# Optimization experiments

Measured on AMD Instinct MI355X. Metric: run time of the kernel, lower is better.

The kernel has to match this reference:

```python
import jax, jax.numpy as jnp
import numpy as np

H, N, D, K = 4, 512, 64, 64  # n_heads, node_num, d_model, sparse_k
TEMP = 0.5
EPS = 1e-10


def setup_inputs() -> dict:
    key = jax.random.key(0)
    k1, k2, k3 = jax.random.split(key, 3)
    feats = jax.random.normal(k1, (H, N, D), jnp.float32)
    # torch Linear init ~ U(-1/sqrt(fan_in), 1/sqrt(fan_in)); Gaussian scale is fine for a baseline
    W_out = jax.random.normal(k2, (2 * D, D), jnp.float32) * (1.0 / np.sqrt(2 * D))
    b_out = jnp.zeros((D,), jnp.float32)
    W_cat = jax.random.normal(k3, (D, 2), jnp.float32) * (1.0 / np.sqrt(D))
    b_cat = jnp.zeros((2,), jnp.float32)
    return {"feats": feats, "W_out": W_out, "b_out": b_out,
            "W_cat": W_cat, "b_cat": b_cat, "sparse_k": K}


def reference(feats, W_out, b_out, W_cat, b_cat, sparse_k):
    H_, N_, D_ = feats.shape
    E = N_ * N_
    e = jnp.arange(E)
    rec_idx = e // N_   # receiver node of edge e (rel_rec one-hot gather)
    snd_idx = e % N_    # sender node of edge e (rel_send one-hot gather)
    # cat([senders, receivers], -1): [H, E, 2D]
    x = jnp.concatenate([feats[:, snd_idx], feats[:, rec_idx]], axis=-1)
    h = jax.nn.relu(x @ W_out + b_out)          # [H, E, D]
    logits = h @ W_cat + b_cat                  # [H, E, 2]
    # gumbel-softmax, hard (straight-through)
    U = jax.random.uniform(jax.random.key(42), logits.shape, jnp.float32)
    g = -jnp.log(-jnp.log(U + EPS) + EPS)
    y_soft = jax.nn.softmax((logits + g) / TEMP, axis=-1)
    y_hard = jax.nn.one_hot(jnp.argmax(y_soft, axis=-1), 2, dtype=y_soft.dtype)
    y = jax.lax.stop_gradient(y_hard - y_soft) + y_soft
    connection_matrix = y[..., 1].reshape(H_, N_, N_)
    connection_prob = jax.nn.softmax(logits, axis=-1)[..., 1]  # [H, E]
    _, top_idx = jax.lax.top_k(connection_prob, sparse_k)      # top-k over edges per head
    sparse_labels = jnp.zeros_like(connection_prob).at[
        jnp.arange(H_)[:, None], top_idx].set(1.0)
    return connection_matrix, connection_prob, sparse_labels
```

## Files before the change

### kernel.cpp

```cpp
#include <hip/hip_runtime.h>
#include <stdint.h>

#define H_ 4
#define N_ 512
#define D_ 64
#define E_ (N_ * N_)
#define HE_ (H_ * E_)
#define EPS_ 1e-10f

__device__ __forceinline__ void tf2x32(unsigned x0, unsigned x1,
                                       unsigned& o0, unsigned& o1) {
  const unsigned ks0 = 0u;
  const unsigned ks1 = 42u;
  const unsigned ks2 = 0x1BD11BDAu ^ ks0 ^ ks1;
  x0 += ks0; x1 += ks1;
#define TFR(r) { x0 += x1; x1 = (x1 << (r)) | (x1 >> (32 - (r))); x1 ^= x0; }
  TFR(13) TFR(15) TFR(26) TFR(6)
  x0 += ks1; x1 += ks2 + 1u;
  TFR(17) TFR(29) TFR(16) TFR(24)
  x0 += ks2; x1 += ks0 + 2u;
  TFR(13) TFR(15) TFR(26) TFR(6)
  x0 += ks0; x1 += ks1 + 3u;
  TFR(17) TFR(29) TFR(16) TFR(24)
  x0 += ks1; x1 += ks2 + 4u;
  TFR(13) TFR(15) TFR(26) TFR(6)
  x0 += ks2; x1 += ks0 + 5u;
#undef TFR
  o0 = x0; o1 = x1;
}

__device__ __forceinline__ unsigned rng_bits(unsigned j) {
  unsigned a, b;
  tf2x32(0u, j, a, b);
  return a ^ b;
}

__device__ __forceinline__ float u01(unsigned bits) {
  return __uint_as_float((bits >> 9) | 0x3f800000u) - 1.0f;
}

__global__ __launch_bounds__(256) void precompute_ab(
    const float* __restrict__ feats, const float* __restrict__ W_out,
    float* __restrict__ A, float* __restrict__ B,
    unsigned* __restrict__ cnt, unsigned* __restrict__ done) {
  int row = blockIdx.x * 4 + (threadIdx.x >> 6);
  int d = threadIdx.x & 63;
  if (blockIdx.x == 0) {
    if (threadIdx.x < 4) cnt[threadIdx.x] = 0u;
    else if (threadIdx.x < 8) done[threadIdx.x - 4] = 0u;
  }
  __shared__ float f[4][64];
  f[threadIdx.x >> 6][d] = feats[row * D_ + d];
  __syncthreads();
  const float* fr = f[threadIdx.x >> 6];
  float a = 0.f, b = 0.f;
#pragma unroll 8
  for (int k = 0; k < D_; ++k) {
    float fv = fr[k];
    a = fmaf(fv, W_out[k * D_ + d], a);
    b = fmaf(fv, W_out[(k + D_) * D_ + d], b);
  }
  A[row * D_ + d] = a;
  B[row * D_ + d] = b;
}

__global__ __launch_bounds__(256, 4) void edge_kernel(
    const float* __restrict__ A, const float* __restrict__ B,
    const float* __restrict__ b_out, const float* __restrict__ W_cat,
    const float* __restrict__ b_cat, float* __restrict__ out,
    unsigned long long* __restrict__ blockmax) {
  __shared__ __align__(16) float Ash[64][68];
  __shared__ __align__(16) float Bsh[16][64];
  __shared__ float4 bsh4[16];
  __shared__ float4 wc4[32];
  __shared__ float bc2[2];
  __shared__ unsigned long long wmax[4];

  const int t = threadIdx.x;
  const int h = blockIdx.z;
  const int snd_base = blockIdx.x * 64;
  const int rec_base = blockIdx.y * 16;

  {
    const float4* A4 = (const float4*)(A + (h * N_ + snd_base) * D_);
    for (int i = t; i < 1024; i += 256)
      *(float4*)&Ash[i >> 4][(i & 15) << 2] = A4[i];
    const float4* B4 = (const float4*)(B + (h * N_ + rec_base) * D_);
    *(float4*)&Bsh[t >> 4][(t & 15) << 2] = B4[t];
  }
  if (t < 16) bsh4[t] = ((const float4*)b_out)[t];
  else if (t < 48) wc4[t - 16] = ((const float4*)W_cat)[t - 16];
  else if (t == 48) { bc2[0] = b_cat[0]; bc2[1] = b_cat[1]; }
  __syncthreads();

  const int s = t & 63;
  const int rg = (t >> 6) * 4;

  float l0[4], l1[4];
#pragma unroll
  for (int r = 0; r < 4; ++r) { l0[r] = 0.f; l1[r] = 0.f; }

#pragma unroll
  for (int d4 = 0; d4 < 16; ++d4) {
    const float4 a0 = *(const float4*)&Ash[s][d4 << 2];
    const float4 bd = bsh4[d4];
    const float4 wA = wc4[2 * d4];
    const float4 wB = wc4[2 * d4 + 1];
#pragma unroll
    for (int r = 0; r < 4; ++r) {
      const float4 bv = *(const float4*)&Bsh[rg + r][d4 << 2];
      float t0;
      t0 = fmaxf((a0.x + bv.x) + bd.x, 0.f);
      l0[r] = fmaf(t0, wA.x, l0[r]); l1[r] = fmaf(t0, wA.y, l1[r]);
      t0 = fmaxf((a0.y + bv.y) + bd.y, 0.f);
      l0[r] = fmaf(t0, wA.z, l0[r]); l1[r] = fmaf(t0, wA.w, l1[r]);
      t0 = fmaxf((a0.z + bv.z) + bd.z, 0.f);
      l0[r] = fmaf(t0, wB.x, l0[r]); l1[r] = fmaf(t0, wB.y, l1[r]);
      t0 = fmaxf((a0.w + bv.w) + bd.w, 0.f);
      l0[r] = fmaf(t0, wB.z, l0[r]); l1[r] = fmaf(t0, wB.w, l1[r]);
    }
  }

  unsigned long long mk = 0ull;
#pragma unroll
  for (int r = 0; r < 4; ++r) {
    float L0 = l0[r] + bc2[0];
    float L1 = l1[r] + bc2[1];
    const unsigned snd = (unsigned)(snd_base + s);
    const unsigned rec = (unsigned)(rec_base + rg + r);
    const unsigned e = rec * (unsigned)N_ + snd;
    const unsigned base = ((unsigned)h << 18) + e;
    const unsigned j0 = base * 2u;

    float uu0 = u01(rng_bits(j0));
    float uu1 = u01(rng_bits(j0 + 1u));
    float g0 = -logf(-logf(uu0 + EPS_) + EPS_);
    float g1 = -logf(-logf(uu1 + EPS_) + EPS_);

    float cm = ((L1 + g1) > (L0 + g0)) ? 1.0f : 0.0f;

    float lm = fmaxf(L0, L1);
    float p0 = expf(L0 - lm), p1 = expf(L1 - lm);
    float pr = p1 / (p0 + p1);

    out[base] = cm;
    out[HE_ + base] = pr;

    unsigned long long key =
        ((unsigned long long)__float_as_uint(pr) << 32) | (unsigned)(~e);
    mk = key > mk ? key : mk;
  }

#pragma unroll
  for (int off = 32; off; off >>= 1) {
    unsigned long long o = __shfl_xor(mk, off, 64);
    mk = o > mk ? o : mk;
  }
  if ((t & 63) == 0) wmax[t >> 6] = mk;
  __syncthreads();
  if (t == 0) {
    unsigned long long m = wmax[0];
#pragma unroll
    for (int i = 1; i < 4; ++i) m = wmax[i] > m ? wmax[i] : m;
    blockmax[h * 256 + blockIdx.y * gridDim.x + blockIdx.x] = m;
  }
}

__global__ __launch_bounds__(512) void topk_fused(
    const float* __restrict__ prob, const unsigned long long* __restrict__ blockmax,
    unsigned* __restrict__ cnt, unsigned* __restrict__ done,
    unsigned long long* __restrict__ cand, float* __restrict__ sparse) {
  __shared__ unsigned long long keys[512];
  __shared__ unsigned long long thrS;
  __shared__ unsigned tkS;
  const int t = threadIdx.x, h = blockIdx.y, blk = blockIdx.x;

  if (t < 256) keys[t] = blockmax[h * 256 + t];
  __syncthreads();
  if (t < 256) {
    unsigned long long my = keys[t];
    int rank = 0;
    for (int j = 0; j < 256; ++j) rank += (keys[j] > my);
    if (rank == 63) thrS = my;
  }
  __syncthreads();
  const unsigned long long thr = thrS;

  const unsigned seg = (unsigned)blk * 4096u;
  {
    float4* sp4 = (float4*)(sparse + (unsigned)h * E_ + seg);
    const float4 z = make_float4(0.f, 0.f, 0.f, 0.f);
#pragma unroll
    for (int i = 0; i < 2; ++i) sp4[t + i * 512] = z;
  }
#pragma unroll
  for (int i = 0; i < 2; ++i) {
    const unsigned e0 = seg + (unsigned)i * 2048u + (unsigned)t * 4u;
    float4 p = *(const float4*)(prob + (unsigned)h * E_ + e0);
    float pv[4] = {p.x, p.y, p.z, p.w};
#pragma unroll
    for (int k2 = 0; k2 < 4; ++k2) {
      unsigned e = e0 + (unsigned)k2;
      unsigned long long key =
          ((unsigned long long)__float_as_uint(pv[k2]) << 32) | (unsigned)(~e);
      if (key >= thr) {
        unsigned pos = atomicAdd(&cnt[h], 1u);
        if (pos < 512u) cand[h * 512 + pos] = key;
      }
    }
  }
  __syncthreads();
  if (t == 0) { __threadfence(); tkS = atomicAdd(&done[h], 1u); }
  __syncthreads();

  if (tkS == 63u) {
    if (t == 0) __threadfence();
    __syncthreads();
    unsigned n = atomicAdd(&cnt[h], 0u);
    if (n > 512u) n = 512u;
    unsigned long long my = (t < (int)n) ? cand[h * 512 + t] : 0ull;
    keys[t] = my;
    __syncthreads();
    int rank = 0;
#pragma unroll 8
    for (int j = 0; j < 512; ++j) rank += (keys[j] > my);
    if (my != 0ull && rank < 64) {
      unsigned e = ~(unsigned)(my & 0xFFFFFFFFull);
      if (e < (unsigned)E_) sparse[(unsigned)h * E_ + e] = 1.0f;
    }
  }
}

extern "C" void kernel_launch(void* const* d_in, const int* in_sizes, int n_in,
                              void* d_out, int out_size, void* d_ws, size_t ws_size,
                              hipStream_t stream) {
  const float* feats = (const float*)d_in[0];
  const float* W_out = (const float*)d_in[1];
  const float* b_out = (const float*)d_in[2];
  const float* W_cat = (const float*)d_in[3];
  const float* b_cat = (const float*)d_in[4];
  float* out = (float*)d_out;

  float* A = (float*)d_ws;
  float* B = A + H_ * N_ * D_;
  unsigned long long* blockmax = (unsigned long long*)(B + H_ * N_ * D_);
  unsigned long long* cand = blockmax + H_ * 256;
  unsigned* cnt = (unsigned*)(cand + H_ * 512);
  unsigned* done = cnt + H_;

  precompute_ab<<<dim3(H_ * N_ / 4), dim3(256), 0, stream>>>(feats, W_out, A, B,
                                                             cnt, done);
  edge_kernel<<<dim3(N_ / 64, N_ / 16, H_), dim3(256), 0, stream>>>(
      A, B, b_out, W_cat, b_cat, out, blockmax);
  topk_fused<<<dim3(64, H_), dim3(512), 0, stream>>>(out + HE_, blockmax, cnt,
                                                     done, cand, out + 2 * HE_);
}
```

Before: 112.1 us.

## Split edge kernel into logits pass and separate Gumbel/softmax pass

Breaks the fused edge kernel into two kernels. The first computes the two logits per edge and writes them to an 8 MB workspace buffer. The second reads them back and does the Threefry RNG, Gumbel noise, softmax, output stores and per-block max reduction with 1024-thread blocks. This likely aims to separate the FMA-heavy stage from the transcendental/RNG-heavy stage so each gets better occupancy and coalesced stores. In exchange it adds a global round trip of the logits and one more kernel launch.

```diff
diff --git a/kernel.cpp b/kernel.cpp
--- a/kernel.cpp
+++ b/kernel.cpp
@@ -64,17 +64,15 @@
   B[row * D_ + d] = b;
 }
 
-__global__ __launch_bounds__(256, 4) void edge_kernel(
+__global__ __launch_bounds__(256, 4) void logits_kernel(
     const float* __restrict__ A, const float* __restrict__ B,
     const float* __restrict__ b_out, const float* __restrict__ W_cat,
-    const float* __restrict__ b_cat, float* __restrict__ out,
-    unsigned long long* __restrict__ blockmax) {
+    const float* __restrict__ b_cat, float2* __restrict__ Lp) {
   __shared__ __align__(16) float Ash[64][68];
   __shared__ __align__(16) float Bsh[16][64];
   __shared__ float4 bsh4[16];
   __shared__ float4 wc4[32];
   __shared__ float bc2[2];
-  __shared__ unsigned long long wmax[4];
 
   const int t = threadIdx.x;
   const int h = blockIdx.z;
@@ -121,36 +119,46 @@
     }
   }
 
-  unsigned long long mk = 0ull;
 #pragma unroll
   for (int r = 0; r < 4; ++r) {
-    float L0 = l0[r] + bc2[0];
-    float L1 = l1[r] + bc2[1];
-    const unsigned snd = (unsigned)(snd_base + s);
-    const unsigned rec = (unsigned)(rec_base + rg + r);
-    const unsigned e = rec * (unsigned)N_ + snd;
-    const unsigned base = ((unsigned)h << 18) + e;
-    const unsigned j0 = base * 2u;
-
-    float uu0 = u01(rng_bits(j0));
-    float uu1 = u01(rng_bits(j0 + 1u));
-    float g0 = -logf(-logf(uu0 + EPS_) + EPS_);
-    float g1 = -logf(-logf(uu1 + EPS_) + EPS_);
-
-    float cm = ((L1 + g1) > (L0 + g0)) ? 1.0f : 0.0f;
-
-    float lm = fmaxf(L0, L1);
-    float p0 = expf(L0 - lm), p1 = expf(L1 - lm);
-    float pr = p1 / (p0 + p1);
-
-    out[base] = cm;
-    out[HE_ + base] = pr;
-
-    unsigned long long key =
-        ((unsigned long long)__float_as_uint(pr) << 32) | (unsigned)(~e);
-    mk = key > mk ? key : mk;
-  }
-
+    const float L0 = l0[r] + bc2[0];
+    const float L1 = l1[r] + bc2[1];
+    const unsigned e = (unsigned)(rec_base + rg + r) * (unsigned)N_ +
+                       (unsigned)(snd_base + s);
+    Lp[((unsigned)h << 18) + e] = make_float2(L0, L1);
+  }
+}
+
+__global__ __launch_bounds__(1024, 8) void gumbel_kernel(
+    const float2* __restrict__ Lp, float* __restrict__ out,
+    unsigned long long* __restrict__ blockmax) {
+  __shared__ unsigned long long wmax[16];
+  const int t = threadIdx.x;
+  const unsigned h = blockIdx.y;
+  const unsigned e = (unsigned)blockIdx.x * 1024u + (unsigned)t;
+  const unsigned base = (h << 18) + e;
+
+  const float2 lp = Lp[base];
+  const float L0 = lp.x;
+  const float L1 = lp.y;
+  const unsigned j0 = base * 2u;
+
+  float uu0 = u01(rng_bits(j0));
+  float uu1 = u01(rng_bits(j0 + 1u));
+  float g0 = -logf(-logf(uu0 + EPS_) + EPS_);
+  float g1 = -logf(-logf(uu1 + EPS_) + EPS_);
+
+  float cm = ((L1 + g1) > (L0 + g0)) ? 1.0f : 0.0f;
+
+  float lm = fmaxf(L0, L1);
+  float p0 = expf(L0 - lm), p1 = expf(L1 - lm);
+  float pr = p1 / (p0 + p1);
+
+  out[base] = cm;
+  out[HE_ + base] = pr;
+
+  unsigned long long mk =
+      ((unsigned long long)__float_as_uint(pr) << 32) | (unsigned)(~e);
 #pragma unroll
   for (int off = 32; off; off >>= 1) {
     unsigned long long o = __shfl_xor(mk, off, 64);
@@ -161,8 +169,8 @@
   if (t == 0) {
     unsigned long long m = wmax[0];
 #pragma unroll
-    for (int i = 1; i < 4; ++i) m = wmax[i] > m ? wmax[i] : m;
-    blockmax[h * 256 + blockIdx.y * gridDim.x + blockIdx.x] = m;
+    for (int i = 1; i < 16; ++i) m = wmax[i] > m ? wmax[i] : m;
+    blockmax[h * 256 + blockIdx.x] = m;
   }
 }
 
@@ -243,15 +251,18 @@
 
   float* A = (float*)d_ws;
   float* B = A + H_ * N_ * D_;
-  unsigned long long* blockmax = (unsigned long long*)(B + H_ * N_ * D_);
+  float2* Lp = (float2*)(B + H_ * N_ * D_);
+  unsigned long long* blockmax = (unsigned long long*)(Lp + HE_);
   unsigned long long* cand = blockmax + H_ * 256;
   unsigned* cnt = (unsigned*)(cand + H_ * 512);
   unsigned* done = cnt + H_;
 
   precompute_ab<<<dim3(H_ * N_ / 4), dim3(256), 0, stream>>>(feats, W_out, A, B,
                                                              cnt, done);
-  edge_kernel<<<dim3(N_ / 64, N_ / 16, H_), dim3(256), 0, stream>>>(
-      A, B, b_out, W_cat, b_cat, out, blockmax);
+  logits_kernel<<<dim3(N_ / 64, N_ / 16, H_), dim3(256), 0, stream>>>(
+      A, B, b_out, W_cat, b_cat, Lp);
+  gumbel_kernel<<<dim3(E_ / 1024, H_), dim3(1024), 0, stream>>>(Lp, out,
+                                                                blockmax);
   topk_fused<<<dim3(64, H_), dim3(512), 0, stream>>>(out + HE_, blockmax, cnt,
                                                      done, cand, out + 2 * HE_);
 }
```

New measurement: 114.6 us. 1.02x slower.

## Fuse the three launches into one cooperative kernel with grid barriers

Applied to the files above, without the earlier changes.

Replaces the precompute, edge and top-k launches with a single cooperative mega-kernel of 1024 workgroups. Phases are separated by a custom grid barrier built on 16 spread-out atomic counters with sleep polling. The goal is to remove per-launch overhead and gaps between kernels, and the zeroing of sparse labels now overlaps with the A/B precompute. In exchange it adds a memset launch and grid-wide barrier latency, and depends on all 1024 blocks being co-resident; if the cooperative launch fails it falls back to the old three-kernel path.

```diff
diff --git a/kernel.cpp b/kernel.cpp
--- a/kernel.cpp
+++ b/kernel.cpp
@@ -7,6 +7,7 @@
 #define E_ (N_ * N_)
 #define HE_ (H_ * E_)
 #define EPS_ 1e-10f
+#define NWG_ 1024ull
 
 __device__ __forceinline__ void tf2x32(unsigned x0, unsigned x1,
                                        unsigned& o0, unsigned& o1) {
@@ -39,6 +40,217 @@
   return __uint_as_float((bits >> 9) | 0x3f800000u) - 1.0f;
 }
 
+#define GBAR(PH)                                                          \
+  do {                                                                    \
+    __syncthreads();                                                      \
+    if (t == 0) {                                                         \
+      __threadfence();                                                    \
+      atomicAdd(&bar[(bl & 15) << 4], 1ull);                              \
+      const unsigned long long _tgt = (unsigned long long)(PH)*NWG_;      \
+      for (long _i = 0; _i < 2000000L; ++_i) {                            \
+        unsigned long long _s = 0ull;                                     \
+        _Pragma("unroll")                                                 \
+        for (int _k = 0; _k < 16; ++_k)                                   \
+          _s += __hip_atomic_load(&bar[_k << 4], __ATOMIC_RELAXED,        \
+                                  __HIP_MEMORY_SCOPE_AGENT);              \
+        if (_s >= _tgt) break;                                            \
+        __builtin_amdgcn_s_sleep(4);                                      \
+      }                                                                   \
+      __threadfence();                                                    \
+    }                                                                     \
+    __syncthreads();                                                      \
+  } while (0)
+
+__global__ __launch_bounds__(256, 4) void mega_kernel(
+    const float* __restrict__ feats, const float* __restrict__ W_out,
+    const float* __restrict__ b_out, const float* __restrict__ W_cat,
+    const float* __restrict__ b_cat, float* __restrict__ out,
+    float* __restrict__ A, float* __restrict__ B,
+    unsigned long long* __restrict__ blockmax,
+    unsigned long long* __restrict__ cand, unsigned* __restrict__ cnt,
+    unsigned long long* __restrict__ bar) {
+  __shared__ __align__(16) float Ash[64][68];
+  __shared__ __align__(16) float Bsh[16][64];
+  __shared__ float4 bsh4[16];
+  __shared__ float4 wc4[32];
+  __shared__ float bc2[2];
+  __shared__ unsigned long long wmax[4];
+  __shared__ unsigned long long thrS;
+
+  const int t = threadIdx.x;
+  const int bl = blockIdx.x;
+  const int bx = bl & 7, by = (bl >> 3) & 31, h = bl >> 8;
+  const int snd_base = bx * 64;
+  const int rec_base = by * 16;
+
+  if (bl == 0 && t < 4) cnt[t] = 0u;
+  {
+    ((float4*)(out + 2 * HE_ + ((unsigned)h << 18) + (unsigned)(bl & 255) * 1024u))[t] =
+        make_float4(0.f, 0.f, 0.f, 0.f);
+
+    const int g = t >> 6;
+    const int d = t & 63;
+    const int row = bl * 2 + (g & 1);
+    float* fsh = &Ash[0][0];
+    if (g < 2) fsh[(g << 6) + d] = feats[row * D_ + d];
+    __syncthreads();
+    if (g < 2) {
+      const float* fr = &fsh[g << 6];
+      float a = 0.f, b = 0.f;
+#pragma unroll 8
+      for (int k = 0; k < D_; ++k) {
+        float fv = fr[k];
+        a = fmaf(fv, W_out[k * D_ + d], a);
+        b = fmaf(fv, W_out[(k + D_) * D_ + d], b);
+      }
+      A[row * D_ + d] = a;
+      B[row * D_ + d] = b;
+    }
+  }
+  GBAR(1);
+
+  {
+    const float4* A4 = (const float4*)(A + (h * N_ + snd_base) * D_);
+    for (int i = t; i < 1024; i += 256)
+      *(float4*)&Ash[i >> 4][(i & 15) << 2] = A4[i];
+    const float4* B4 = (const float4*)(B + (h * N_ + rec_base) * D_);
+    *(float4*)&Bsh[t >> 4][(t & 15) << 2] = B4[t];
+  }
+  if (t < 16) bsh4[t] = ((const float4*)b_out)[t];
+  else if (t < 48) wc4[t - 16] = ((const float4*)W_cat)[t - 16];
+  else if (t == 48) { bc2[0] = b_cat[0]; bc2[1] = b_cat[1]; }
+  __syncthreads();
+
+  const int s = t & 63;
+  const int rg = (t >> 6) * 4;
+
+  float l0[4], l1[4];
+#pragma unroll
+  for (int r = 0; r < 4; ++r) { l0[r] = 0.f; l1[r] = 0.f; }
+
+#pragma unroll
+  for (int d4 = 0; d4 < 16; ++d4) {
+    const float4 a0 = *(const float4*)&Ash[s][d4 << 2];
+    const float4 bd = bsh4[d4];
+    const float4 wA = wc4[2 * d4];
+    const float4 wB = wc4[2 * d4 + 1];
+#pragma unroll
+    for (int r = 0; r < 4; ++r) {
+      const float4 bv = *(const float4*)&Bsh[rg + r][d4 << 2];
+      float t0;
+      t0 = fmaxf((a0.x + bv.x) + bd.x, 0.f);
+      l0[r] = fmaf(t0, wA.x, l0[r]); l1[r] = fmaf(t0, wA.y, l1[r]);
+      t0 = fmaxf((a0.y + bv.y) + bd.y, 0.f);
+      l0[r] = fmaf(t0, wA.z, l0[r]); l1[r] = fmaf(t0, wA.w, l1[r]);
+      t0 = fmaxf((a0.z + bv.z) + bd.z, 0.f);
+      l0[r] = fmaf(t0, wB.x, l0[r]); l1[r] = fmaf(t0, wB.y, l1[r]);
+      t0 = fmaxf((a0.w + bv.w) + bd.w, 0.f);
+      l0[r] = fmaf(t0, wB.z, l0[r]); l1[r] = fmaf(t0, wB.w, l1[r]);
+    }
+  }
+
+  unsigned long long mk = 0ull;
+#pragma unroll
+  for (int r = 0; r < 4; ++r) {
+    float L0 = l0[r] + bc2[0];
+    float L1 = l1[r] + bc2[1];
+    const unsigned snd = (unsigned)(snd_base + s);
+    const unsigned rec = (unsigned)(rec_base + rg + r);
+    const unsigned e = rec * (unsigned)N_ + snd;
+    const unsigned base = ((unsigned)h << 18) + e;
+    const unsigned j0 = base * 2u;
+
+    float uu0 = u01(rng_bits(j0));
+    float uu1 = u01(rng_bits(j0 + 1u));
+    float g0 = -logf(-logf(uu0 + EPS_) + EPS_);
+    float g1 = -logf(-logf(uu1 + EPS_) + EPS_);
+
+    float cm = ((L1 + g1) > (L0 + g0)) ? 1.0f : 0.0f;
+
+    float lm = fmaxf(L0, L1);
+    float p0 = expf(L0 - lm), p1 = expf(L1 - lm);
+    float pr = p1 / (p0 + p1);
+
+    out[base] = cm;
+    out[HE_ + base] = pr;
+
+    unsigned long long key =
+        ((unsigned long long)__float_as_uint(pr) << 32) | (unsigned)(~e);
+    mk = key > mk ? key : mk;
+  }
+
+#pragma unroll
+  for (int off = 32; off; off >>= 1) {
+    unsigned long long o = __shfl_xor(mk, off, 64);
+    mk = o > mk ? o : mk;
+  }
+  if ((t & 63) == 0) wmax[t >> 6] = mk;
+  __syncthreads();
+  if (t == 0) {
+    unsigned long long m = wmax[0];
+#pragma unroll
+    for (int i = 1; i < 4; ++i) m = wmax[i] > m ? wmax[i] : m;
+    blockmax[h * 256 + (bl & 255)] = m;
+  }
+  GBAR(2);
+
+  {
+    unsigned long long* keyS = (unsigned long long*)&Ash[0][0];
+    keyS[t] = blockmax[h * 256 + t];
+    __syncthreads();
+    {
+      unsigned long long my = keyS[t];
+      int rank = 0;
+      for (int j = 0; j < 256; ++j) rank += (keyS[j] > my);
+      if (rank == 63) thrS = my;
+    }
+    __syncthreads();
+    const unsigned long long thr = thrS;
+
+    const unsigned e0 = (unsigned)(bl & 255) * 1024u + (unsigned)t * 4u;
+    float4 p = *(const float4*)(out + HE_ + ((unsigned)h << 18) + e0);
+    float pv[4] = {p.x, p.y, p.z, p.w};
+#pragma unroll
+    for (int k2 = 0; k2 < 4; ++k2) {
+      unsigned e = e0 + (unsigned)k2;
+      unsigned long long key =
+          ((unsigned long long)__float_as_uint(pv[k2]) << 32) | (unsigned)(~e);
+      if (key >= thr) {
+        unsigned pos = atomicAdd(&cnt[h], 1u);
+        if (pos < 512u) cand[h * 512 + pos] = key;
+      }
+    }
+  }
+  GBAR(3);
+
+  if (bl < 4) {
+    const int h3 = bl;
+    unsigned n = atomicAdd(&cnt[h3], 0u);
+    if (n > 512u) n = 512u;
+    unsigned long long* k512 = (unsigned long long*)&Ash[0][0];
+    unsigned long long m0 = (t < (int)n) ? cand[h3 * 512 + t] : 0ull;
+    unsigned long long m1 = (t + 256 < (int)n) ? cand[h3 * 512 + t + 256] : 0ull;
+    k512[t] = m0;
+    k512[t + 256] = m1;
+    __syncthreads();
+    int r0 = 0, r1 = 0;
+#pragma unroll 8
+    for (int j = 0; j < 512; ++j) {
+      unsigned long long kj = k512[j];
+      r0 += (kj > m0);
+      r1 += (kj > m1);
+    }
+    if (m0 != 0ull && r0 < 64) {
+      unsigned e = ~(unsigned)(m0 & 0xFFFFFFFFull);
+      if (e < (unsigned)E_) out[2 * HE_ + ((unsigned)h3 << 18) + e] = 1.0f;
+    }
+    if (m1 != 0ull && r1 < 64) {
+      unsigned e = ~(unsigned)(m1 & 0xFFFFFFFFull);
+      if (e < (unsigned)E_) out[2 * HE_ + ((unsigned)h3 << 18) + e] = 1.0f;
+    }
+  }
+}
+
 __global__ __launch_bounds__(256) void precompute_ab(
     const float* __restrict__ feats, const float* __restrict__ W_out,
     float* __restrict__ A, float* __restrict__ B,
@@ -247,11 +459,23 @@
   unsigned long long* cand = blockmax + H_ * 256;
   unsigned* cnt = (unsigned*)(cand + H_ * 512);
   unsigned* done = cnt + H_;
-
-  precompute_ab<<<dim3(H_ * N_ / 4), dim3(256), 0, stream>>>(feats, W_out, A, B,
-                                                             cnt, done);
-  edge_kernel<<<dim3(N_ / 64, N_ / 16, H_), dim3(256), 0, stream>>>(
-      A, B, b_out, W_cat, b_cat, out, blockmax);
-  topk_fused<<<dim3(64, H_), dim3(512), 0, stream>>>(out + HE_, blockmax, cnt,
-                                                     done, cand, out + 2 * HE_);
-}
+  unsigned long long* bar = (unsigned long long*)((char*)d_ws + (4u << 20));
+
+  hipMemsetAsync((void*)bar, 0, 16 * 16 * sizeof(unsigned long long), stream);
+
+  void* args[] = {(void*)&feats, (void*)&W_out, (void*)&b_out, (void*)&W_cat,
+                  (void*)&b_cat, (void*)&out,   (void*)&A,     (void*)&B,
+                  (void*)&blockmax, (void*)&cand, (void*)&cnt, (void*)&bar};
+  hipError_t err = hipLaunchCooperativeKernel(
+      reinterpret_cast<void*>(mega_kernel), dim3(1024), dim3(256), args, 0,
+      stream);
+  if (err != hipSuccess) {
+    precompute_ab<<<dim3(H_ * N_ / 4), dim3(256), 0, stream>>>(feats, W_out, A,
+                                                               B, cnt, done);
+    edge_kernel<<<dim3(N_ / 64, N_ / 16, H_), dim3(256), 0, stream>>>(
+        A, B, b_out, W_cat, b_cat, out, blockmax);
+    topk_fused<<<dim3(64, H_), dim3(512), 0, stream>>>(out + HE_, blockmax,
+                                                       cnt, done, cand,
+                                                       out + 2 * HE_);
+  }
+}
```

Measured after the change: 287.7 us. 157% more time.

## Fuse top-k selection into edge kernel using last-block-per-head completion

Applied to the files above, without the earlier changes.

Drops the separate top-k launch. The edge kernel now zeroes its slice of sparse_labels, and the last block to finish each head (found through an atomic done counter) computes the threshold from the per-block maxima. That same block then scans all of the head's probabilities for candidates and ranks them in shared memory. The edge tile is halved to 32 senders, giving more, smaller blocks and finer-grained block maxima. In exchange, the full 1 MB probability scan per head now runs in a single block as a serial tail, instead of being spread across 64 blocks.

```diff
diff --git a/kernel.cpp b/kernel.cpp
--- a/kernel.cpp
+++ b/kernel.cpp
@@ -42,13 +42,10 @@
 __global__ __launch_bounds__(256) void precompute_ab(
     const float* __restrict__ feats, const float* __restrict__ W_out,
     float* __restrict__ A, float* __restrict__ B,
-    unsigned* __restrict__ cnt, unsigned* __restrict__ done) {
+    unsigned* __restrict__ done) {
   int row = blockIdx.x * 4 + (threadIdx.x >> 6);
   int d = threadIdx.x & 63;
-  if (blockIdx.x == 0) {
-    if (threadIdx.x < 4) cnt[threadIdx.x] = 0u;
-    else if (threadIdx.x < 8) done[threadIdx.x - 4] = 0u;
-  }
+  if (blockIdx.x == 0 && threadIdx.x < 4) done[threadIdx.x] = 0u;
   __shared__ float f[4][64];
   f[threadIdx.x >> 6][d] = feats[row * D_ + d];
   __syncthreads();
@@ -64,26 +61,29 @@
   B[row * D_ + d] = b;
 }
 
-__global__ __launch_bounds__(256, 4) void edge_kernel(
+__global__ __launch_bounds__(256, 4) void edge_topk(
     const float* __restrict__ A, const float* __restrict__ B,
     const float* __restrict__ b_out, const float* __restrict__ W_cat,
     const float* __restrict__ b_cat, float* __restrict__ out,
-    unsigned long long* __restrict__ blockmax) {
-  __shared__ __align__(16) float Ash[64][68];
+    unsigned long long* __restrict__ blockmax, unsigned* __restrict__ done) {
+  __shared__ __align__(16) float Ash[32][68];
   __shared__ __align__(16) float Bsh[16][64];
   __shared__ float4 bsh4[16];
   __shared__ float4 wc4[32];
   __shared__ float bc2[2];
   __shared__ unsigned long long wmax[4];
+  __shared__ unsigned long long thrS;
+  __shared__ unsigned tkS, cntS;
 
   const int t = threadIdx.x;
   const int h = blockIdx.z;
-  const int snd_base = blockIdx.x * 64;
+  const int snd_base = blockIdx.x * 32;
   const int rec_base = blockIdx.y * 16;
+  const int chunk = blockIdx.y * 16 + blockIdx.x;
 
   {
     const float4* A4 = (const float4*)(A + (h * N_ + snd_base) * D_);
-    for (int i = t; i < 1024; i += 256)
+    for (int i = t; i < 512; i += 256)
       *(float4*)&Ash[i >> 4][(i & 15) << 2] = A4[i];
     const float4* B4 = (const float4*)(B + (h * N_ + rec_base) * D_);
     *(float4*)&Bsh[t >> 4][(t & 15) << 2] = B4[t];
@@ -93,12 +93,12 @@
   else if (t == 48) { bc2[0] = b_cat[0]; bc2[1] = b_cat[1]; }
   __syncthreads();
 
-  const int s = t & 63;
-  const int rg = (t >> 6) * 4;
-
-  float l0[4], l1[4];
-#pragma unroll
-  for (int r = 0; r < 4; ++r) { l0[r] = 0.f; l1[r] = 0.f; }
+  const int s = t & 31;
+  const int rg = (t >> 5) * 2;
+
+  float l0[2], l1[2];
+#pragma unroll
+  for (int r = 0; r < 2; ++r) { l0[r] = 0.f; l1[r] = 0.f; }
 
 #pragma unroll
   for (int d4 = 0; d4 < 16; ++d4) {
@@ -107,7 +107,7 @@
     const float4 wA = wc4[2 * d4];
     const float4 wB = wc4[2 * d4 + 1];
 #pragma unroll
-    for (int r = 0; r < 4; ++r) {
+    for (int r = 0; r < 2; ++r) {
       const float4 bv = *(const float4*)&Bsh[rg + r][d4 << 2];
       float t0;
       t0 = fmaxf((a0.x + bv.x) + bd.x, 0.f);
@@ -123,7 +123,7 @@
 
   unsigned long long mk = 0ull;
 #pragma unroll
-  for (int r = 0; r < 4; ++r) {
+  for (int r = 0; r < 2; ++r) {
     float L0 = l0[r] + bc2[0];
     float L1 = l1[r] + bc2[1];
     const unsigned snd = (unsigned)(snd_base + s);
@@ -151,6 +151,12 @@
     mk = key > mk ? key : mk;
   }
 
+  {
+    float4* sp = (float4*)(out + 2 * HE_ + ((unsigned)h << 18) +
+                           (unsigned)chunk * 512u);
+    if (t < 128) sp[t] = make_float4(0.f, 0.f, 0.f, 0.f);
+  }
+
 #pragma unroll
   for (int off = 32; off; off >>= 1) {
     unsigned long long o = __shfl_xor(mk, off, 64);
@@ -162,71 +168,78 @@
     unsigned long long m = wmax[0];
 #pragma unroll
     for (int i = 1; i < 4; ++i) m = wmax[i] > m ? wmax[i] : m;
-    blockmax[h * 256 + blockIdx.y * gridDim.x + blockIdx.x] = m;
-  }
-}
-
-__global__ __launch_bounds__(512) void topk_fused(
-    const float* __restrict__ prob, const unsigned long long* __restrict__ blockmax,
-    unsigned* __restrict__ cnt, unsigned* __restrict__ done,
-    unsigned long long* __restrict__ cand, float* __restrict__ sparse) {
-  __shared__ unsigned long long keys[512];
-  __shared__ unsigned long long thrS;
-  __shared__ unsigned tkS;
-  const int t = threadIdx.x, h = blockIdx.y, blk = blockIdx.x;
-
-  if (t < 256) keys[t] = blockmax[h * 256 + t];
-  __syncthreads();
-  if (t < 256) {
-    unsigned long long my = keys[t];
-    int rank = 0;
-    for (int j = 0; j < 256; ++j) rank += (keys[j] > my);
-    if (rank == 63) thrS = my;
+    blockmax[h * 512 + chunk] = m;
+  }
+
+  __syncthreads();
+  if (t == 0) { __threadfence(); tkS = atomicAdd(&done[h], 1u); }
+  __syncthreads();
+  if (tkS != 511u) return;
+
+  if (t == 0) __threadfence();
+  __syncthreads();
+
+  unsigned long long* keyS = (unsigned long long*)&Ash[0][0];
+  unsigned long long* candS = keyS + 512;
+  keyS[t] = blockmax[h * 512 + t];
+  keyS[t + 256] = blockmax[h * 512 + 256 + t];
+  if (t == 0) cntS = 0u;
+  __syncthreads();
+  {
+    unsigned long long k0 = keyS[t], k1 = keyS[t + 256];
+    int r0 = 0, r1 = 0;
+    for (int j = 0; j < 512; ++j) {
+      unsigned long long kj = keyS[j];
+      r0 += (kj > k0);
+      r1 += (kj > k1);
+    }
+    if (r0 == 63) thrS = k0;
+    if (r1 == 63) thrS = k1;
   }
   __syncthreads();
   const unsigned long long thr = thrS;
 
-  const unsigned seg = (unsigned)blk * 4096u;
-  {
-    float4* sp4 = (float4*)(sparse + (unsigned)h * E_ + seg);
-    const float4 z = make_float4(0.f, 0.f, 0.f, 0.f);
-#pragma unroll
-    for (int i = 0; i < 2; ++i) sp4[t + i * 512] = z;
-  }
-#pragma unroll
-  for (int i = 0; i < 2; ++i) {
-    const unsigned e0 = seg + (unsigned)i * 2048u + (unsigned)t * 4u;
-    float4 p = *(const float4*)(prob + (unsigned)h * E_ + e0);
-    float pv[4] = {p.x, p.y, p.z, p.w};
-#pragma unroll
-    for (int k2 = 0; k2 < 4; ++k2) {
-      unsigned e = e0 + (unsigned)k2;
-      unsigned long long key =
-          ((unsigned long long)__float_as_uint(pv[k2]) << 32) | (unsigned)(~e);
-      if (key >= thr) {
-        unsigned pos = atomicAdd(&cnt[h], 1u);
-        if (pos < 512u) cand[h * 512 + pos] = key;
+  {
+    const float4* P4 = (const float4*)(out + HE_ + ((unsigned)h << 18));
+    for (int i = 0; i < 256; ++i) {
+      const unsigned idx = (unsigned)i * 256u + (unsigned)t;
+      float4 p = P4[idx];
+      const unsigned e0 = idx * 4u;
+      float pv[4] = {p.x, p.y, p.z, p.w};
+#pragma unroll
+      for (int k2 = 0; k2 < 4; ++k2) {
+        unsigned long long key =
+            ((unsigned long long)__float_as_uint(pv[k2]) << 32) |
+            (unsigned)(~(e0 + (unsigned)k2));
+        if (key >= thr) {
+          unsigned pos = atomicAdd(&cntS, 1u);
+          if (pos < 512u) candS[pos] = key;
+        }
       }
     }
   }
   __syncthreads();
-  if (t == 0) { __threadfence(); tkS = atomicAdd(&done[h], 1u); }
-  __syncthreads();
-
-  if (tkS == 63u) {
-    if (t == 0) __threadfence();
-    __syncthreads();
-    unsigned n = atomicAdd(&cnt[h], 0u);
-    if (n > 512u) n = 512u;
-    unsigned long long my = (t < (int)n) ? cand[h * 512 + t] : 0ull;
-    keys[t] = my;
-    __syncthreads();
-    int rank = 0;
+  unsigned n = cntS;
+  if (n > 512u) n = 512u;
+  if (t >= (int)n) candS[t] = 0ull;
+  if (t + 256 >= (int)n) candS[t + 256] = 0ull;
+  __syncthreads();
+  {
+    unsigned long long m0 = candS[t], m1 = candS[t + 256];
+    int r0 = 0, r1 = 0;
 #pragma unroll 8
-    for (int j = 0; j < 512; ++j) rank += (keys[j] > my);
-    if (my != 0ull && rank < 64) {
-      unsigned e = ~(unsigned)(my & 0xFFFFFFFFull);
-      if (e < (unsigned)E_) sparse[(unsigned)h * E_ + e] = 1.0f;
+    for (int j = 0; j < 512; ++j) {
+      unsigned long long kj = candS[j];
+      r0 += (kj > m0);
+      r1 += (kj > m1);
+    }
+    if (m0 != 0ull && r0 < 64) {
+      unsigned e = ~(unsigned)(m0 & 0xFFFFFFFFull);
+      if (e < (unsigned)E_) out[2 * HE_ + ((unsigned)h << 18) + e] = 1.0f;
+    }
+    if (m1 != 0ull && r1 < 64) {
+      unsigned e = ~(unsigned)(m1 & 0xFFFFFFFFull);
+      if (e < (unsigned)E_) out[2 * HE_ + ((unsigned)h << 18) + e] = 1.0f;
     }
   }
 }
@@ -244,14 +257,10 @@
   float* A = (float*)d_ws;
   float* B = A + H_ * N_ * D_;
   unsigned long long* blockmax = (unsigned long long*)(B + H_ * N_ * D_);
-  unsigned long long* cand = blockmax + H_ * 256;
-  unsigned* cnt = (unsigned*)(cand + H_ * 512);
-  unsigned* done = cnt + H_;
+  unsigned* done = (unsigned*)(blockmax + H_ * 512);
 
   precompute_ab<<<dim3(H_ * N_ / 4), dim3(256), 0, stream>>>(feats, W_out, A, B,
-                                                             cnt, done);
-  edge_kernel<<<dim3(N_ / 64, N_ / 16, H_), dim3(256), 0, stream>>>(
-      A, B, b_out, W_cat, b_cat, out, blockmax);
-  topk_fused<<<dim3(64, H_), dim3(512), 0, stream>>>(out + HE_, blockmax, cnt,
-                                                     done, cand, out + 2 * HE_);
-}
+                                                             done);
+  edge_topk<<<dim3(N_ / 32, N_ / 16, H_), dim3(256), 0, stream>>>(
+      A, B, b_out, W_cat, b_cat, out, blockmax, done);
+}
```

After: 252.5 us. 125% more time.
